# Kernel tuning notes

Hardware: AMD Instinct MI355X
Metric: run time of the kernel (lower is better)

Reference implementation:

```python
import jax, jax.numpy as jnp
import numpy as np


def setup_inputs() -> dict:
    key = jax.random.key(0)
    k1, k2, k3, k4, k5 = jax.random.split(key, 5)
    B, T, H_enc, H_dec, A = 64, 2048, 512, 512, 512
    scale_enc = float(np.sqrt(2.0 / (H_enc + A)))  # xavier_uniform-ish scale
    scale_dec = float(np.sqrt(2.0 / (H_dec + A)))
    scale_v = float(np.sqrt(2.0 / (A + 1)))
    return {
        "encoder_outputs": jax.random.normal(k1, (B, T, H_enc), dtype=jnp.float32),
        "decoder_hidden": jax.random.normal(k2, (B, H_dec), dtype=jnp.float32),
        "W_enc": jax.random.normal(k3, (A, H_enc), dtype=jnp.float32) * scale_enc,
        "W_dec": jax.random.normal(k4, (A, H_dec), dtype=jnp.float32) * scale_dec,
        "V": jax.random.normal(k5, (1, A), dtype=jnp.float32) * scale_v,
    }


def reference(encoder_outputs, decoder_hidden, W_enc, W_dec, V):
    # enc_proj: [B,T,A]; dec_proj: [B,1,A] broadcast-added
    enc_proj = jnp.einsum("bth,ah->bta", encoder_outputs, W_enc)
    dec_proj = jnp.einsum("bh,ah->ba", decoder_hidden, W_dec)[:, None, :]
    energy = jnp.tanh(enc_proj + dec_proj)                      # [B,T,A]
    scores = jnp.einsum("bta,a->bt", energy, V[0])              # [B,T]
    attention_weights = jax.nn.softmax(scores, axis=1)          # [B,T]
    context_vector = jnp.einsum("bt,bth->bh", attention_weights, encoder_outputs)
    return context_vector, attention_weights
```

## Files before the change

kernel.cpp:

```cpp
#include <hip/hip_runtime.h>

#define B_ 64
#define T_ 2048
#define H_ 512
#define A_ 512

typedef unsigned short u16;
typedef __attribute__((ext_vector_type(8))) short bf16x8;
typedef __attribute__((ext_vector_type(4))) float f32x4;

__device__ __forceinline__ unsigned cvtpk(float lo, float hi) {
  unsigned d;
  asm("v_cvt_pk_bf16_f32 %0, %1, %2" : "=v"(d) : "v"(lo), "v"(hi));
  return d;
}

__device__ __forceinline__ float bf2f(u16 h) {
  return __uint_as_float(((unsigned)h) << 16);
}

__device__ __forceinline__ float fast_tanh(float x) {
  float e2;
  asm("v_exp_f32 %0, %1" : "=v"(e2) : "v"(x * 2.8853900817779268f));
  return 1.0f - 2.0f * __builtin_amdgcn_rcpf(e2 + 1.0f);
}

#define BAR_LDS() asm volatile("s_waitcnt lgkmcnt(0)\n\ts_barrier" ::: "memory")

__global__ void k_prep(const float* __restrict__ W, u16* __restrict__ wsB,
                       const float* __restrict__ dec, const float* __restrict__ Wd,
                       float* __restrict__ dp) {
  __shared__ float dl[H_];
  int tid = threadIdx.x;
  int bx = blockIdx.x;
  if (bx < 128) {
    int u = bx * 256 + tid;
    int a = u >> 6;
    int hq = u & 63;
    int ks = hq >> 2;
    int q = hq & 3;
    const float4* src = (const float4*)(W + a * H_ + hq * 8);
    float4 x0 = src[0], x1 = src[1];
    uint4 pk;
    pk.x = cvtpk(x0.x, x0.y);
    pk.y = cvtpk(x0.z, x0.w);
    pk.z = cvtpk(x1.x, x1.y);
    pk.w = cvtpk(x1.z, x1.w);
    int dst = ks * 2048 + (a >> 4) * 64 + q * 16 + (a & 15);
    ((uint4*)wsB)[dst] = pk;
  } else {
    int e = bx - 128;
    int b = e >> 3;
    int a0 = (e & 7) * 64;
    dl[tid] = dec[b * H_ + tid];
    dl[tid + 256] = dec[b * H_ + tid + 256];
    __syncthreads();
    int al = tid >> 2, p = tid & 3;
    const float4* wr = (const float4*)(Wd + (a0 + al) * H_ + p * 128);
    const float4* dv = (const float4*)(dl + p * 128);
    float s = 0.f;
#pragma unroll 8
    for (int i = 0; i < 32; ++i) {
      float4 w4 = wr[i], d4 = dv[i];
      s += w4.x * d4.x + w4.y * d4.y + w4.z * d4.z + w4.w * d4.w;
    }
    s += __shfl_xor(s, 1);
    s += __shfl_xor(s, 2);
    if (p == 0) dp[b * H_ + a0 + al] = s;
  }
}

__launch_bounds__(512, 4)
__global__ void k_scores(const float* __restrict__ enc, const u16* __restrict__ wsB,
                         const float* __restrict__ dpj, const float* __restrict__ V,
                         float* __restrict__ scores, float* __restrict__ part,
                         float* __restrict__ mz) {
  __shared__ __attribute__((aligned(16))) u16 Ab[64 * 512];
  __shared__ float red[8][64];
  int tid = threadIdx.x;
  int w = tid >> 6, l = tid & 63;
  int q = l >> 4, r = l & 15;
  int m0 = blockIdx.x * 64;
  int b = m0 >> 11;

  int rem = tid & 255;
  int sm = rem >> 6, sq = (rem >> 4) & 3, sr = rem & 15;
  const float* ab = enc + (size_t)(m0 + sm * 16 + sr) * H_ + (tid >> 8) * 32 + sq * 8;

  float vv[4], dd[4];
  const float* db = dpj + b * A_;
#pragma unroll
  for (int n = 0; n < 4; ++n) {
    int col = w * 64 + n * 16 + r;
    vv[n] = V[col];
    dd[n] = db[col];
  }

  const bf16x8* bfrag = (const bf16x8*)wsB;

#define LOADC(P, c)                                                     \
  { P##0 = *((const float4*)(ab + (2 * (c)) * 64));                     \
    P##1 = *((const float4*)(ab + (2 * (c)) * 64 + 4));                 \
    P##2 = *((const float4*)(ab + (2 * (c) + 1) * 64));                 \
    P##3 = *((const float4*)(ab + (2 * (c) + 1) * 64 + 4)); }
#define WRITEC(P, c)                                                    \
  { uint4 k0, k1;                                                       \
    k0.x = cvtpk((P##0).x, (P##0).y); k0.y = cvtpk((P##0).z, (P##0).w); \
    k0.z = cvtpk((P##1).x, (P##1).y); k0.w = cvtpk((P##1).z, (P##1).w); \
    k1.x = cvtpk((P##2).x, (P##2).y); k1.y = cvtpk((P##2).z, (P##2).w); \
    k1.z = cvtpk((P##3).x, (P##3).y); k1.w = cvtpk((P##3).z, (P##3).w); \
    ((uint4*)Ab)[(2 * (c)) * 512 + tid] = k0;                           \
    ((uint4*)Ab)[(2 * (c) + 1) * 512 + tid] = k1; }
#define LOADB2(dst, ks, nb)                                             \
  { dst[0] = bfrag[(ks) * 2048 + (w * 4 + (nb)) * 64 + l];              \
    dst[1] = bfrag[(ks) * 2048 + (w * 4 + (nb) + 1) * 64 + l]; }
#define MFMA8(af, bb)                                                   \
  { __builtin_amdgcn_s_setprio(1);                                      \
    _Pragma("unroll") for (int m = 0; m < 4; ++m)                       \
      _Pragma("unroll") for (int n = 0; n < 2; ++n)                     \
        acc[m][n] = __builtin_amdgcn_mfma_f32_16x16x32_bf16(            \
            af[m], bb[n], acc[m][n], 0, 0, 0);                          \
    __builtin_amdgcn_s_setprio(0); }
#define KSTEP2(ks, scur, spre, PF, nb)                                  \
  { if (PF) LOADB2(spre, (ks) + 2, nb)                                  \
    bf16x8 af[4];                                                       \
    _Pragma("unroll") for (int m = 0; m < 4; ++m)                       \
      af[m] = *((const bf16x8*)&Ab[((ks) * 256 + m * 64 + l) * 8]);     \
    MFMA8(af, scur) }
#define CHUNK2(c, PF3, nb)                                              \
  { KSTEP2(4 * (c), s0, s2, true, nb)                                   \
    KSTEP2(4 * (c) + 1, s1, s3, true, nb)                               \
    KSTEP2(4 * (c) + 2, s2, s0, PF3, nb)                                \
    KSTEP2(4 * (c) + 3, s3, s1, PF3, nb) }
#define ACC_SP(nb)                                                      \
  _Pragma("unroll") for (int n = 0; n < 2; ++n) {                       \
    _Pragma("unroll") for (int m = 0; m < 4; ++m)                       \
      _Pragma("unroll") for (int j = 0; j < 4; ++j)                     \
        sp[m * 4 + j] = fmaf(vv[(nb) + n],                              \
                             fast_tanh(acc[m][n][j] + dd[(nb) + n]),    \
                             sp[m * 4 + j]);                            \
  }

  f32x4 acc[4][2];
#pragma unroll
  for (int m = 0; m < 4; ++m)
#pragma unroll
    for (int n = 0; n < 2; ++n) acc[m][n] = (f32x4){0.f, 0.f, 0.f, 0.f};
  float sp[16];
#pragma unroll
  for (int i = 0; i < 16; ++i) sp[i] = 0.f;

  float4 pa0, pa1, pa2, pa3;
  bf16x8 s0[2], s1[2], s2[2], s3[2];

  LOADB2(s0, 0, 0)
  LOADB2(s1, 1, 0)
  LOADC(pa, 0)
  WRITEC(pa, 0)
  BAR_LDS();
  LOADC(pa, 1)
  CHUNK2(0, true, 0)
  WRITEC(pa, 1)
  BAR_LDS();
  LOADC(pa, 2)
  CHUNK2(1, true, 0)
  WRITEC(pa, 2)
  BAR_LDS();
  LOADC(pa, 3)
  CHUNK2(2, true, 0)
  WRITEC(pa, 3)
  BAR_LDS();
  CHUNK2(3, false, 0)

  ACC_SP(0)
#pragma unroll
  for (int m = 0; m < 4; ++m)
#pragma unroll
    for (int n = 0; n < 2; ++n) acc[m][n] = (f32x4){0.f, 0.f, 0.f, 0.f};

  LOADB2(s0, 0, 2)
  LOADB2(s1, 1, 2)
  CHUNK2(0, true, 2)
  CHUNK2(1, true, 2)
  CHUNK2(2, true, 2)
  CHUNK2(3, false, 2)

  ACC_SP(2)

#pragma unroll
  for (int st = 0; st < 4; ++st) {
    const int s = 1 << st;
    const int cnt = 16 >> (st + 1);
    bool hi = (r & s) != 0;
#pragma unroll
    for (int i = 0; i < cnt; ++i) {
      float a = hi ? sp[i + cnt] : sp[i];
      float bs = hi ? sp[i] : sp[i + cnt];
      sp[i] = a + __shfl_xor(bs, s);
    }
  }
  {
    int i4 = ((r & 1) << 3) | ((r & 2) << 1) | ((r & 4) >> 1) | ((r & 8) >> 3);
    BAR_LDS();
    red[w][(i4 >> 2) * 16 + q * 4 + (i4 & 3)] = sp[0];
  }
  BAR_LDS();

  float s_ = 0.f;
#pragma unroll
  for (int ww = 0; ww < 8; ++ww) s_ += red[ww][l];
  if (w == 0) scores[m0 + l] = s_;
  float mx = s_;
#pragma unroll
  for (int off = 1; off <= 32; off <<= 1) mx = fmaxf(mx, __shfl_xor(mx, off));
  float e = __expf(s_ - mx);
  float Z = e;
#pragma unroll
  for (int off = 1; off <= 32; off <<= 1) Z += __shfl_xor(Z, off);
  if (tid == 0) {
    mz[blockIdx.x * 2] = mx;
    mz[blockIdx.x * 2 + 1] = Z;
  }
  float em[4];
#pragma unroll
  for (int m = 0; m < 4; ++m) em[m] = __shfl(e, m * 16 + r);

  {
    float pv0[8], pv1[8];
#pragma unroll
    for (int j = 0; j < 8; ++j) { pv0[j] = 0.f; pv1[j] = 0.f; }
#pragma unroll
    for (int ksl = 0; ksl < 2; ++ksl) {
      int ks_ = 2 * w + ksl;
#pragma unroll
      for (int m = 0; m < 4; ++m) {
        uint4 pk = ((const uint4*)Ab)[ks_ * 256 + m * 64 + l];
        float er = em[m];
        float v0 = bf2f((u16)(pk.x & 0xffff)), v1 = bf2f((u16)(pk.x >> 16));
        float v2 = bf2f((u16)(pk.y & 0xffff)), v3 = bf2f((u16)(pk.y >> 16));
        float v4 = bf2f((u16)(pk.z & 0xffff)), v5 = bf2f((u16)(pk.z >> 16));
        float v6 = bf2f((u16)(pk.w & 0xffff)), v7 = bf2f((u16)(pk.w >> 16));
        if (ksl == 0) {
          pv0[0] = fmaf(er, v0, pv0[0]); pv0[1] = fmaf(er, v1, pv0[1]);
          pv0[2] = fmaf(er, v2, pv0[2]); pv0[3] = fmaf(er, v3, pv0[3]);
          pv0[4] = fmaf(er, v4, pv0[4]); pv0[5] = fmaf(er, v5, pv0[5]);
          pv0[6] = fmaf(er, v6, pv0[6]); pv0[7] = fmaf(er, v7, pv0[7]);
        } else {
          pv1[0] = fmaf(er, v0, pv1[0]); pv1[1] = fmaf(er, v1, pv1[1]);
          pv1[2] = fmaf(er, v2, pv1[2]); pv1[3] = fmaf(er, v3, pv1[3]);
          pv1[4] = fmaf(er, v4, pv1[4]); pv1[5] = fmaf(er, v5, pv1[5]);
          pv1[6] = fmaf(er, v6, pv1[6]); pv1[7] = fmaf(er, v7, pv1[7]);
        }
      }
    }
#pragma unroll
    for (int st = 0; st < 3; ++st) {
      const int s = 1 << st;
      const int cnt = 8 >> (st + 1);
      bool hi = (r & s) != 0;
#pragma unroll
      for (int i = 0; i < cnt; ++i) {
        float a0 = hi ? pv0[i + cnt] : pv0[i];
        float b0 = hi ? pv0[i] : pv0[i + cnt];
        pv0[i] = a0 + __shfl_xor(b0, s);
        float a1 = hi ? pv1[i + cnt] : pv1[i];
        float b1 = hi ? pv1[i] : pv1[i + cnt];
        pv1[i] = a1 + __shfl_xor(b1, s);
      }
    }
    bool h8 = (r & 8) != 0;
    float va = h8 ? pv1[0] : pv0[0];
    float vb = h8 ? pv0[0] : pv1[0];
    float ov = va + __shfl_xor(vb, 8);
    int g3 = ((r & 1) << 2) | (r & 2) | ((r & 4) >> 2);
    int col = w * 64 + (h8 ? 32 : 0) + q * 8 + g3;
    part[(size_t)blockIdx.x * 512 + col] = ov;
  }
#undef LOADC
#undef WRITEC
#undef LOADB2
#undef MFMA8
#undef KSTEP2
#undef CHUNK2
#undef ACC_SP
}

__global__ void k_softmax(const float* __restrict__ scores, float* __restrict__ wts) {
  __shared__ float rm[4], rs[4];
  int b = blockIdx.x, tid = threadIdx.x;
  float s[8];
#pragma unroll
  for (int i = 0; i < 8; ++i) s[i] = scores[b * T_ + i * 256 + tid];
  float mx = s[0];
#pragma unroll
  for (int i = 1; i < 8; ++i) mx = fmaxf(mx, s[i]);
#pragma unroll
  for (int off = 1; off <= 32; off <<= 1) mx = fmaxf(mx, __shfl_xor(mx, off));
  if ((tid & 63) == 0) rm[tid >> 6] = mx;
  __syncthreads();
  mx = fmaxf(fmaxf(rm[0], rm[1]), fmaxf(rm[2], rm[3]));
  float ex[8], se = 0.f;
#pragma unroll
  for (int i = 0; i < 8; ++i) { ex[i] = __expf(s[i] - mx); se += ex[i]; }
#pragma unroll
  for (int off = 1; off <= 32; off <<= 1) se += __shfl_xor(se, off);
  if ((tid & 63) == 0) rs[tid >> 6] = se;
  __syncthreads();
  se = rs[0] + rs[1] + rs[2] + rs[3];
  float inv = 1.0f / se;
#pragma unroll
  for (int i = 0; i < 8; ++i) wts[b * T_ + i * 256 + tid] = ex[i] * inv;
}

__global__ void k_ctx_comb(const float* __restrict__ part, const float* __restrict__ mz,
                           float* __restrict__ ctx) {
  __shared__ float sM[32], sZ[32];
  int b = blockIdx.x, tid = threadIdx.x;
  if (tid < 32) {
    sM[tid] = mz[(b * 32 + tid) * 2];
    sZ[tid] = mz[(b * 32 + tid) * 2 + 1];
  }
  __syncthreads();
  float M = sM[0];
#pragma unroll
  for (int i = 1; i < 32; ++i) M = fmaxf(M, sM[i]);
  float denom = 0.f;
#pragma unroll
  for (int i = 0; i < 32; ++i) denom += sZ[i] * __expf(sM[i] - M);
  float s = 0.f;
#pragma unroll
  for (int i = 0; i < 32; ++i)
    s += part[((size_t)b * 32 + i) * 512 + tid] * __expf(sM[i] - M);
  ctx[b * 512 + tid] = s / denom;
}

extern "C" void kernel_launch(void* const* d_in, const int* in_sizes, int n_in,
                              void* d_out, int out_size, void* d_ws, size_t ws_size,
                              hipStream_t stream) {
  const float* enc  = (const float*)d_in[0];
  const float* dec  = (const float*)d_in[1];
  const float* Wenc = (const float*)d_in[2];
  const float* Wdec = (const float*)d_in[3];
  const float* V    = (const float*)d_in[4];
  float* out = (float*)d_out;
  char* ws = (char*)d_ws;

  u16* wsB      = (u16*)ws;
  float* dpj    = (float*)(ws + 512 * 1024);
  float* scores = (float*)(ws + 640 * 1024);
  float* part   = (float*)(ws + 1152 * 1024);
  float* mz     = (float*)(ws + 1152 * 1024 + 4 * 1024 * 1024);

  float* ctx = out;
  float* wts = out + B_ * H_;

  hipLaunchKernelGGL(k_prep, dim3(640), dim3(256), 0, stream, Wenc, wsB, dec, Wdec, dpj);
  hipLaunchKernelGGL(k_scores, dim3(2048), dim3(512), 0, stream, enc, wsB, dpj, V,
                     scores, part, mz);
  hipLaunchKernelGGL(k_softmax, dim3(64), dim3(256), 0, stream, scores, wts);
  hipLaunchKernelGGL(k_ctx_comb, dim3(64), dim3(512), 0, stream, part, mz, ctx);
}
```

Measured before the change: 115.4 us.

## Fuse softmax with context combine, retile decoder projection, double-buffer enc loads

Merges the softmax and context-combine kernels into one post kernel, removing a launch and its dependency gap. Reworks the decoder projection in k_prep so each block stages 32 decoder rows in LDS and computes 4 batches per thread, giving each W_dec element more reuse and needing fewer blocks. In k_scores it adds a second set of prefetch registers so two encoder chunks are in flight at once. The extra registers may lower occupancy in the main kernel, and the larger LDS in k_prep may reduce its occupancy.

```diff
diff --git a/kernel.cpp b/kernel.cpp
--- a/kernel.cpp
+++ b/kernel.cpp
@@ -30,7 +30,7 @@
 __global__ void k_prep(const float* __restrict__ W, u16* __restrict__ wsB,
                        const float* __restrict__ dec, const float* __restrict__ Wd,
                        float* __restrict__ dp) {
-  __shared__ float dl[H_];
+  __shared__ float dl[32 * 512];
   int tid = threadIdx.x;
   int bx = blockIdx.x;
   if (bx < 128) {
@@ -50,23 +50,34 @@
     ((uint4*)wsB)[dst] = pk;
   } else {
     int e = bx - 128;
-    int b = e >> 3;
-    int a0 = (e & 7) * 64;
-    dl[tid] = dec[b * H_ + tid];
-    dl[tid + 256] = dec[b * H_ + tid + 256];
+    int ac = e >> 1, bh = e & 1;
+    int a0 = ac * 32;
+    const float4* dsrc = (const float4*)(dec + bh * 32 * H_);
+    float4* dl4 = (float4*)dl;
+#pragma unroll
+    for (int i = 0; i < 16; ++i) dl4[i * 256 + tid] = dsrc[i * 256 + tid];
     __syncthreads();
-    int al = tid >> 2, p = tid & 3;
-    const float4* wr = (const float4*)(Wd + (a0 + al) * H_ + p * 128);
-    const float4* dv = (const float4*)(dl + p * 128);
-    float s = 0.f;
+    int al = tid >> 3, bg = tid & 7;
+    int a = a0 + al;
+    const float4* wr = (const float4*)(Wd + (size_t)a * H_);
+    float p0 = 0.f, p1 = 0.f, p2 = 0.f, p3 = 0.f;
 #pragma unroll 8
-    for (int i = 0; i < 32; ++i) {
-      float4 w4 = wr[i], d4 = dv[i];
-      s += w4.x * d4.x + w4.y * d4.y + w4.z * d4.z + w4.w * d4.w;
+    for (int i = 0; i < 128; ++i) {
+      float4 w4 = wr[i];
+      float4 d0 = dl4[(bg * 4 + 0) * 128 + i];
+      float4 d1 = dl4[(bg * 4 + 1) * 128 + i];
+      float4 d2 = dl4[(bg * 4 + 2) * 128 + i];
+      float4 d3 = dl4[(bg * 4 + 3) * 128 + i];
+      p0 += w4.x * d0.x + w4.y * d0.y + w4.z * d0.z + w4.w * d0.w;
+      p1 += w4.x * d1.x + w4.y * d1.y + w4.z * d1.z + w4.w * d1.w;
+      p2 += w4.x * d2.x + w4.y * d2.y + w4.z * d2.z + w4.w * d2.w;
+      p3 += w4.x * d3.x + w4.y * d3.y + w4.z * d3.z + w4.w * d3.w;
     }
-    s += __shfl_xor(s, 1);
-    s += __shfl_xor(s, 2);
-    if (p == 0) dp[b * H_ + a0 + al] = s;
+    int b0 = bh * 32 + bg * 4;
+    dp[(b0 + 0) * H_ + a] = p0;
+    dp[(b0 + 1) * H_ + a] = p1;
+    dp[(b0 + 2) * H_ + a] = p2;
+    dp[(b0 + 3) * H_ + a] = p3;
   }
 }
 
@@ -150,25 +161,25 @@
 #pragma unroll
   for (int i = 0; i < 16; ++i) sp[i] = 0.f;
 
-  float4 pa0, pa1, pa2, pa3;
+  float4 pa0, pa1, pa2, pa3, pb0, pb1, pb2, pb3;
   bf16x8 s0[2], s1[2], s2[2], s3[2];
 
   LOADB2(s0, 0, 0)
   LOADB2(s1, 1, 0)
   LOADC(pa, 0)
+  LOADC(pb, 1)
   WRITEC(pa, 0)
   BAR_LDS();
-  LOADC(pa, 1)
+  LOADC(pa, 2)
   CHUNK2(0, true, 0)
-  WRITEC(pa, 1)
-  BAR_LDS();
-  LOADC(pa, 2)
+  WRITEC(pb, 1)
+  BAR_LDS();
+  LOADC(pb, 3)
   CHUNK2(1, true, 0)
   WRITEC(pa, 2)
   BAR_LDS();
-  LOADC(pa, 3)
   CHUNK2(2, true, 0)
-  WRITEC(pa, 3)
+  WRITEC(pb, 3)
   BAR_LDS();
   CHUNK2(3, false, 0)
 
@@ -285,53 +296,50 @@
 #undef ACC_SP
 }
 
-__global__ void k_softmax(const float* __restrict__ scores, float* __restrict__ wts) {
-  __shared__ float rm[4], rs[4];
-  int b = blockIdx.x, tid = threadIdx.x;
-  float s[8];
-#pragma unroll
-  for (int i = 0; i < 8; ++i) s[i] = scores[b * T_ + i * 256 + tid];
-  float mx = s[0];
-#pragma unroll
-  for (int i = 1; i < 8; ++i) mx = fmaxf(mx, s[i]);
-#pragma unroll
-  for (int off = 1; off <= 32; off <<= 1) mx = fmaxf(mx, __shfl_xor(mx, off));
-  if ((tid & 63) == 0) rm[tid >> 6] = mx;
-  __syncthreads();
-  mx = fmaxf(fmaxf(rm[0], rm[1]), fmaxf(rm[2], rm[3]));
-  float ex[8], se = 0.f;
-#pragma unroll
-  for (int i = 0; i < 8; ++i) { ex[i] = __expf(s[i] - mx); se += ex[i]; }
-#pragma unroll
-  for (int off = 1; off <= 32; off <<= 1) se += __shfl_xor(se, off);
-  if ((tid & 63) == 0) rs[tid >> 6] = se;
-  __syncthreads();
-  se = rs[0] + rs[1] + rs[2] + rs[3];
-  float inv = 1.0f / se;
-#pragma unroll
-  for (int i = 0; i < 8; ++i) wts[b * T_ + i * 256 + tid] = ex[i] * inv;
-}
-
-__global__ void k_ctx_comb(const float* __restrict__ part, const float* __restrict__ mz,
-                           float* __restrict__ ctx) {
-  __shared__ float sM[32], sZ[32];
+__global__ void k_post(const float* __restrict__ scores, const float* __restrict__ part,
+                       const float* __restrict__ mz, float* __restrict__ wts,
+                       float* __restrict__ ctx) {
+  __shared__ float rm[8], rs[8], sM[32], sZ[32];
   int b = blockIdx.x, tid = threadIdx.x;
   if (tid < 32) {
     sM[tid] = mz[(b * 32 + tid) * 2];
     sZ[tid] = mz[(b * 32 + tid) * 2 + 1];
   }
+  float s[4];
+#pragma unroll
+  for (int i = 0; i < 4; ++i) s[i] = scores[b * T_ + i * 512 + tid];
+  float mx = fmaxf(fmaxf(s[0], s[1]), fmaxf(s[2], s[3]));
+#pragma unroll
+  for (int off = 1; off <= 32; off <<= 1) mx = fmaxf(mx, __shfl_xor(mx, off));
+  if ((tid & 63) == 0) rm[tid >> 6] = mx;
   __syncthreads();
+#pragma unroll
+  for (int i = 0; i < 8; ++i) mx = fmaxf(mx, rm[i]);
+  float ex[4], se = 0.f;
+#pragma unroll
+  for (int i = 0; i < 4; ++i) { ex[i] = __expf(s[i] - mx); se += ex[i]; }
+#pragma unroll
+  for (int off = 1; off <= 32; off <<= 1) se += __shfl_xor(se, off);
+  if ((tid & 63) == 0) rs[tid >> 6] = se;
+  __syncthreads();
+  se = 0.f;
+#pragma unroll
+  for (int i = 0; i < 8; ++i) se += rs[i];
+  float inv = 1.0f / se;
+#pragma unroll
+  for (int i = 0; i < 4; ++i) wts[b * T_ + i * 512 + tid] = ex[i] * inv;
+
   float M = sM[0];
 #pragma unroll
   for (int i = 1; i < 32; ++i) M = fmaxf(M, sM[i]);
   float denom = 0.f;
 #pragma unroll
   for (int i = 0; i < 32; ++i) denom += sZ[i] * __expf(sM[i] - M);
-  float s = 0.f;
+  float acc = 0.f;
 #pragma unroll
   for (int i = 0; i < 32; ++i)
-    s += part[((size_t)b * 32 + i) * 512 + tid] * __expf(sM[i] - M);
-  ctx[b * 512 + tid] = s / denom;
+    acc += part[((size_t)b * 32 + i) * 512 + tid] * __expf(sM[i] - M);
+  ctx[b * 512 + tid] = acc / denom;
 }
 
 extern "C" void kernel_launch(void* const* d_in, const int* in_sizes, int n_in,
@@ -354,9 +362,8 @@
   float* ctx = out;
   float* wts = out + B_ * H_;
 
-  hipLaunchKernelGGL(k_prep, dim3(640), dim3(256), 0, stream, Wenc, wsB, dec, Wdec, dpj);
+  hipLaunchKernelGGL(k_prep, dim3(160), dim3(256), 0, stream, Wenc, wsB, dec, Wdec, dpj);
   hipLaunchKernelGGL(k_scores, dim3(2048), dim3(512), 0, stream, enc, wsB, dpj, V,
                      scores, part, mz);
-  hipLaunchKernelGGL(k_softmax, dim3(64), dim3(256), 0, stream, scores, wts);
-  hipLaunchKernelGGL(k_ctx_comb, dim3(64), dim3(512), 0, stream, part, mz, ctx);
-}
+  hipLaunchKernelGGL(k_post, dim3(64), dim3(512), 0, stream, scores, part, mz, wts, ctx);
+}
```

Measured after the change: 149.0 us, median of 2. 29.1% more time.
